# Kernel tuning notes

Measured on AMD Instinct MI355X. Metric: run time of the kernel, lower is better.

Reference implementation:

```python
import jax, jax.numpy as jnp
import numpy as np

B, S, DM, DC, L, NS = 4, 2048, 2048, 512, 4, 5  # batch, seq, d_model, d_cortical, n_layers, n_settle


def _ln(x, g, b):
    # torch nn.LayerNorm, eps=1e-5
    m = x.mean(-1, keepdims=True)
    v = ((x - m) ** 2).mean(-1, keepdims=True)
    return (x - m) * jax.lax.rsqrt(v + 1e-5) * g + b


def setup_inputs() -> dict:
    key = jax.random.key(0)
    ks = jax.random.split(key, 20)
    f = lambda k, sh: jax.random.normal(k, sh, jnp.float32) * 0.02
    return dict(
        qwen_final_hidden=jax.random.normal(ks[0], (B, S, DM), jnp.float32),
        obs=jax.random.normal(ks[1], (4, B, S, DM), jnp.float32),
        proj_W=f(ks[2], (4, DC, DM)), proj_b=f(ks[3], (4, DC)),
        fuse_W=f(ks[4], (DC, 4 * DC)), fuse_b=f(ks[5], (DC,)),
        up_W=f(ks[6], (L, DC, DC)), up_b=f(ks[7], (L, DC)),
        lateral_W=f(ks[8], (L, DC, DC)), lateral_b=f(ks[9], (L, DC)),
        precision_logit=f(ks[10], (L, DC)),
        ln_g=jnp.ones((L, DC), jnp.float32), ln_b=jnp.zeros((L, DC), jnp.float32),
        down_W=f(ks[11], (L - 1, DC, DC)), down_b=f(ks[12], (L - 1, DC)),
        out1_W=f(ks[13], (DC, DC)), out1_b=f(ks[14], (DC,)),
        out2_W=f(ks[15], (DM, DC)), out2_b=f(ks[16], (DM,)),
    )


def reference(qwen_final_hidden, obs, proj_W, proj_b, fuse_W, fuse_b,
              up_W, up_b, lateral_W, lateral_b, precision_logit,
              ln_g, ln_b, down_W, down_b, out1_W, out1_b, out2_W, out2_b):
    b, s, dm = qwen_final_hidden.shape
    # per-observed-layer input projections, concatenated along features
    proj = jnp.einsum('obsd,ocd->bsoc', obs, proj_W) + proj_b  # (B,S,4,DC)
    cat = proj.reshape(b, s, -1)
    fused = cat @ fuse_W.T + fuse_b                             # (B,S,DC)
    x0 = fused.reshape(b * s, DC)                               # per-token cortical input

    prec = jax.nn.sigmoid(precision_logit)                      # (L,DC)

    # initial bottom-up pass: activations = compress(x)
    acts = []
    x = x0
    for i in range(L):
        x = _ln(x @ up_W[i].T + up_b[i], ln_g[i], ln_b[i])
        acts.append(x)

    # settling iterations
    for _ in range(NS):
        # top-down predictions computed from pre-sweep activations
        preds = [None] * L
        for i in range(L - 1, 0, -1):
            if i < L - 1:  # top layer has no top-down weights
                preds[i - 1] = acts[i] @ down_W[i].T + down_b[i]
        x = x0
        for i in range(L):
            compressed = _ln(x @ up_W[i].T + up_b[i], ln_g[i], ln_b[i])
            target = preds[i] if preds[i] is not None else acts[i]
            werr = (compressed - target) * prec[i]
            lateral = acts[i] @ lateral_W[i].T + lateral_b[i]
            acts[i] = _ln(acts[i] + 0.5 * werr + 0.1 * lateral, ln_g[i], ln_b[i])
            x = acts[i]

    top = acts[-1]
    h = jax.nn.gelu(top @ out1_W.T + out1_b, approximate=False)
    correction = (h @ out2_W.T + out2_b).reshape(b, s, dm)
    return qwen_final_hidden + correction
```

## Files before the change

### kernel.cpp

```cpp
#include <hip/hip_runtime.h>
#include <hip/hip_bf16.h>
#include <math.h>

#define NTOK 8192
#define DMD  2048
#define DCC  512
#define TOKH 4194304

typedef __attribute__((ext_vector_type(8))) short short8;
typedef __attribute__((ext_vector_type(4))) float f32x4;

__device__ inline float bf2f(unsigned short u) {
    union { unsigned int i; float f; } x; x.i = ((unsigned int)u) << 16; return x.f;
}
__device__ inline unsigned short f2bf(float f) {
    union { float f; unsigned int i; } x; x.f = f;
    unsigned int u = x.i;
    return (unsigned short)((u + 0x7fffu + ((u >> 16) & 1u)) >> 16);
}

typedef const __attribute__((address_space(1))) unsigned int* gas1_t;
typedef __attribute__((address_space(3))) unsigned int* las3_t;
__device__ inline void async16(const void* g, void* l) {
    __builtin_amdgcn_global_load_lds(
        (gas1_t)g,
        (las3_t)(unsigned int)(unsigned long long)l, 16, 0, 0);
}

#define VMCNT(N) asm volatile("s_waitcnt vmcnt(" #N ")" ::: "memory")

__global__ __launch_bounds__(256)
void cvt_kernel(const float* __restrict__ s, unsigned short* __restrict__ d, int n4)
{
    for (int i = blockIdx.x * 256 + threadIdx.x; i < n4; i += gridDim.x * 256) {
        float4 v = ((const float4*)s)[i];
        ushort4 o;
        o.x = f2bf(v.x); o.y = f2bf(v.y); o.z = f2bf(v.z); o.w = f2bf(v.w);
        ((ushort4*)d)[i] = o;
    }
}

struct PrepArgs {
    const float* wsrc[6];
    const float* proj_W;
    const float* fuse_W;
    const float* fuse_b;
    const float* proj_b;
    unsigned short* wdst;
    unsigned short* projT;
    float* bp;
};

__global__ __launch_bounds__(256)
void prep_kernel(PrepArgs pa)
{
    __shared__ float t[32][33];
    const int bid = blockIdx.x;
    const int tid = threadIdx.x;

    if (bid < 2048) {
        const int total = 1310720;
        for (int i = bid * 256 + tid; i < total; i += 2048 * 256) {
            const float* sp; int base;
            if      (i <  262144) { sp = pa.wsrc[0]; base = 0;       }
            else if (i <  524288) { sp = pa.wsrc[1]; base = 262144;  }
            else if (i <  786432) { sp = pa.wsrc[2]; base = 524288;  }
            else if (i <  983040) { sp = pa.wsrc[3]; base = 786432;  }
            else if (i < 1048576) { sp = pa.wsrc[4]; base = 983040;  }
            else                  { sp = pa.wsrc[5]; base = 1048576; }
            float4 v = ((const float4*)sp)[i - base];
            ushort4 o;
            o.x = f2bf(v.x); o.y = f2bf(v.y); o.z = f2bf(v.z); o.w = f2bf(v.w);
            ((ushort4*)pa.wdst)[i] = o;
        }
    } else if (bid < 6144) {
        const int b2  = bid - 2048;
        const int o   = b2 >> 10;
        const int rem = b2 & 1023;
        const int jb  = (rem & 63) * 32;
        const int kb  = (rem >> 6) * 32;
        const int r   = tid >> 3;
        const int c4  = (tid & 7) * 4;
        {
            const float* s = pa.proj_W + ((size_t)o * DCC + kb + r) * DMD + jb + c4;
            float4 v = *(const float4*)s;
            t[r][c4+0]=v.x; t[r][c4+1]=v.y; t[r][c4+2]=v.z; t[r][c4+3]=v.w;
        }
        __syncthreads();
        {
            ushort4 u;
            u.x = f2bf(t[c4+0][r]); u.y = f2bf(t[c4+1][r]);
            u.z = f2bf(t[c4+2][r]); u.w = f2bf(t[c4+3][r]);
            *(ushort4*)(pa.projT + ((size_t)o * DMD + jb + r) * DCC + kb + c4) = u;
        }
    } else {
        const int b3  = bid - 6144;
        const int row = b3 * 8 + (tid >> 5);
        const int l32 = tid & 31;
        const float* r = pa.fuse_W + (size_t)row * (4 * DCC) + l32 * 64;
        const float* p = pa.proj_b + l32 * 64;
        float s = 0.f;
        #pragma unroll
        for (int k = 0; k < 64; k += 4) {
            float4 v = *(const float4*)(r + k);
            float4 q = *(const float4*)(p + k);
            s += v.x*q.x + v.y*q.y + v.z*q.z + v.w*q.w;
        }
        #pragma unroll
        for (int off = 16; off; off >>= 1) s += __shfl_xor(s, off, 64);
        if (l32 == 0) pa.bp[row] = s + pa.fuse_b[row];
    }
}

struct GArgs {
    const unsigned short* A[6];
    const unsigned short* W[6];
    const float*          bias[6];
    const float*          add[6];
    void*                 C[6];
};

template<bool OUTF32, bool GELU>
__global__ __launch_bounds__(256)
void gemm16(GArgs ga, int lda, int ldw, int ldadd, int ldc, int K)
{
    __shared__ unsigned short As[3][128 * 32];
    __shared__ unsigned short Bs[3][128 * 32];

    const int z    = blockIdx.z;
    const int tid  = threadIdx.x;
    const int wave = tid >> 6;
    const int lane = tid & 63;

    const int nwg   = gridDim.x * gridDim.y;
    const int bid   = blockIdx.y * gridDim.x + blockIdx.x;
    const int swz   = (bid & 7) * (nwg >> 3) + (bid >> 3);
    const int bn    = (swz % gridDim.x) * 128;
    const int bm    = (swz / gridDim.x) * 128;

    const int wr   = wave >> 1;
    const int wc   = wave & 1;

    const unsigned short* Ap = ga.A[z];
    const unsigned short* Wp = ga.W[z];

    const int lrow = lane >> 2;
    const int lcol = (lane & 3) * 8;
    const int l15  = lane & 15;
    const int lh   = lane >> 4;

    f32x4 acc[4][4] = {};

    const int nsteps = K >> 5;

    auto issue = [&](int buf, int k0) {
        #pragma unroll
        for (int r = 0; r < 2; ++r) {
            int c = wave + r * 4;
            async16(Ap + (size_t)(bm + c * 16 + lrow) * lda + k0 + lcol,
                    &As[buf][c * 512]);
            async16(Wp + (size_t)(bn + c * 16 + lrow) * ldw + k0 + lcol,
                    &Bs[buf][c * 512]);
        }
    };

    issue(0, 0);
    issue(1, 32);

    for (int t = 0; t < nsteps; ++t) {
        const int cur = t % 3;
        if (t < nsteps - 1) VMCNT(4);
        else                VMCNT(0);
        __builtin_amdgcn_s_barrier();
        if (t + 2 < nsteps) issue((t + 2) % 3, (t + 2) * 32);

        short8 af[4], bfr[4];
        #pragma unroll
        for (int i = 0; i < 4; ++i) {
            af[i]  = *(const short8*)&As[cur][(wr * 64 + i * 16 + l15) * 32 + lh * 8];
            bfr[i] = *(const short8*)&Bs[cur][(wc * 64 + i * 16 + l15) * 32 + lh * 8];
        }
        __builtin_amdgcn_s_setprio(1);
        #pragma unroll
        for (int mi = 0; mi < 4; ++mi)
            #pragma unroll
            for (int ni = 0; ni < 4; ++ni)
                acc[mi][ni] = __builtin_amdgcn_mfma_f32_16x16x32_bf16(
                    af[mi], bfr[ni], acc[mi][ni], 0, 0, 0);
        __builtin_amdgcn_s_setprio(0);
    }

    const float* bias = ga.bias[z];
    const float* add  = ga.add[z];
    #pragma unroll
    for (int ni = 0; ni < 4; ++ni) {
        int col = bn + wc * 64 + ni * 16 + l15;
        float bv = bias ? bias[col] : 0.0f;
        #pragma unroll
        for (int mi = 0; mi < 4; ++mi) {
            #pragma unroll
            for (int r = 0; r < 4; ++r) {
                int row = bm + wr * 64 + mi * 16 + lh * 4 + r;
                float vv = acc[mi][ni][r] + bv;
                if (GELU) vv = 0.5f * vv * (1.0f + erff(vv * 0.7071067811865475f));
                if (OUTF32) {
                    if (add) vv += add[(size_t)row * ldadd + col];
                    ((float*)ga.C[z])[(size_t)row * ldc + col] = vv;
                } else {
                    ((unsigned short*)ga.C[z])[(size_t)row * ldc + col] = f2bf(vv);
                }
            }
        }
    }
}

__global__ __launch_bounds__(256)
void x0red(const float* __restrict__ partial, const float* __restrict__ bp,
           unsigned short* __restrict__ x0)
{
    const int i = blockIdx.x * 256 + threadIdx.x;
    float4 a = ((const float4*)partial)[i];
    float4 b = ((const float4*)(partial + TOKH))[i];
    float4 c = ((const float4*)(partial + 2 * (size_t)TOKH))[i];
    float4 d = ((const float4*)(partial + 3 * (size_t)TOKH))[i];
    const int col = (i * 4) & (DCC - 1);
    float4 bv = *(const float4*)(bp + col);
    ushort4 o;
    o.x = f2bf(a.x + b.x + c.x + d.x + bv.x);
    o.y = f2bf(a.y + b.y + c.y + d.y + bv.y);
    o.z = f2bf(a.z + b.z + c.z + d.z + bv.z);
    o.w = f2bf(a.w + b.w + c.w + d.w + bv.w);
    ((ushort4*)x0)[i] = o;
}

__device__ inline int csw(int rl, int col) {
    int s = ((rl >> 2) & 3) ^ (rl & 3);
    return rl * 512 + (col ^ (s << 4));
}

template<int MODE>
__global__ __launch_bounds__(512)
void gemm_fused2(const unsigned short* __restrict__ Ap,
                 const unsigned short* __restrict__ W0,
                 const float* __restrict__ bias0,
                 const float* __restrict__ g0,
                 const float* __restrict__ b0,
                 const unsigned short* a0,
                 const unsigned short* t0,
                 const unsigned short* __restrict__ lat0,
                 const float* __restrict__ logit0,
                 unsigned short* out0,
                 const unsigned short* __restrict__ W1,
                 const float* __restrict__ bias1,
                 const float* __restrict__ g1,
                 const float* __restrict__ b1,
                 const unsigned short* a1,
                 const unsigned short* t1,
                 const unsigned short* __restrict__ lat1,
                 const float* __restrict__ logit1,
                 unsigned short* out1)
{
    __shared__ unsigned short Bs[3][512 * 32];
    __shared__ unsigned short As3[3][32 * 32];
    __shared__ unsigned short xS[32 * 512];
    __shared__ float red[2][8][32];

    const int tid  = threadIdx.x;
    const int wave = tid >> 6;
    const int lane = tid & 63;
    const int lrow = lane >> 2;
    const int lc8  = (lane & 3) * 8;
    const int bm   = blockIdx.x * 32;
    const int l15  = lane & 15;
    const int lh   = lane >> 4;
    const int c0   = lane * 8;

    f32x4 acc[2][4];

    auto ln1_to_xS = [&](const float* bias, const float* g, const float* b) {
        float bv[4], gv[4], bbv[4];
        #pragma unroll
        for (int ni = 0; ni < 4; ++ni) {
            int col = wave * 64 + ni * 16 + l15;
            bv[ni] = bias[col]; gv[ni] = g[col]; bbv[ni] = b[col];
        }
        float ps[2][4], pq[2][4];
        #pragma unroll
        for (int mi = 0; mi < 2; ++mi)
            #pragma unroll
            for (int rr = 0; rr < 4; ++rr) {
                float s = 0.f, q = 0.f;
                #pragma unroll
                for (int ni = 0; ni < 4; ++ni) {
                    float v = acc[mi][ni][rr] + bv[ni];
                    acc[mi][ni][rr] = v;
                    s += v; q += v * v;
                }
                #pragma unroll
                for (int off = 1; off < 16; off <<= 1) {
                    s += __shfl_xor(s, off, 64);
                    q += __shfl_xor(q, off, 64);
                }
                ps[mi][rr] = s; pq[mi][rr] = q;
            }
        if (l15 == 0) {
            #pragma unroll
            for (int mi = 0; mi < 2; ++mi)
                #pragma unroll
                for (int rr = 0; rr < 4; ++rr) {
                    int rl = mi * 16 + lh * 4 + rr;
                    red[0][wave][rl] = ps[mi][rr];
                    red[1][wave][rl] = pq[mi][rr];
                }
        }
        __syncthreads();
        #pragma unroll
        for (int mi = 0; mi < 2; ++mi)
            #pragma unroll
            for (int rr = 0; rr < 4; ++rr) {
                int rl = mi * 16 + lh * 4 + rr;
                float s = 0.f, q = 0.f;
                #pragma unroll
                for (int w = 0; w < 8; ++w) { s += red[0][w][rl]; q += red[1][w][rl]; }
                float m1 = s * (1.0f / DCC);
                float r1 = rsqrtf(q * (1.0f / DCC) - m1 * m1 + 1e-5f);
                #pragma unroll
                for (int ni = 0; ni < 4; ++ni) {
                    int col = wave * 64 + ni * 16 + l15;
                    xS[csw(rl, col)] = f2bf((acc[mi][ni][rr] - m1) * r1 * gv[ni] + bbv[ni]);
                }
            }
        __syncthreads();
    };

    auto phase2 = [&](const unsigned short* a_in, const unsigned short* t_in,
                      const unsigned short* lat_in, const float* g,
                      const float* b, const float* logit,
                      unsigned short* outp, bool keep) {
        if constexpr (MODE == 0) {
            #pragma unroll
            for (int rr = 0; rr < 4; ++rr) {
                const int rl = wave * 4 + rr;
                const size_t gbase = (size_t)(bm + rl) * DCC + c0;
                short8 cm = *(const short8*)&xS[csw(rl, c0)];
                *(short8*)(outp + gbase) = cm;
            }
        } else {
            float gr[8], br[8], pr[8];
            {
                float4 ga = *(const float4*)(g + c0),     gb = *(const float4*)(g + c0 + 4);
                float4 ba = *(const float4*)(b + c0),     bb2 = *(const float4*)(b + c0 + 4);
                float4 pA = *(const float4*)(logit + c0), pB = *(const float4*)(logit + c0 + 4);
                float gt[8] = {ga.x,ga.y,ga.z,ga.w,gb.x,gb.y,gb.z,gb.w};
                float bt[8] = {ba.x,ba.y,ba.z,ba.w,bb2.x,bb2.y,bb2.z,bb2.w};
                float pt[8] = {pA.x,pA.y,pA.z,pA.w,pB.x,pB.y,pB.z,pB.w};
                #pragma unroll
                for (int j = 0; j < 8; ++j) {
                    gr[j] = gt[j]; br[j] = bt[j];
                    pr[j] = 1.0f / (1.0f + __expf(-pt[j]));
                }
            }
            #pragma unroll
            for (int rr = 0; rr < 4; ++rr) {
                const int rl = wave * 4 + rr;
                const size_t gbase = (size_t)(bm + rl) * DCC + c0;
                short8 cm = *(const short8*)&xS[csw(rl, c0)];
                short8 ar = *(const short8*)(a_in + gbase);
                short8 tr = *(const short8*)(t_in + gbase);
                short8 lr = *(const short8*)(lat_in + gbase);
                float tv[8], s = 0.f, q = 0.f;
                #pragma unroll
                for (int j = 0; j < 8; ++j) {
                    float val = bf2f((unsigned short)ar[j])
                              + 0.5f * (bf2f((unsigned short)cm[j]) - bf2f((unsigned short)tr[j])) * pr[j]
                              + 0.1f * bf2f((unsigned short)lr[j]);
                    tv[j] = val; s += val; q += val * val;
                }
                #pragma unroll
                for (int off = 1; off < 64; off <<= 1) {
                    s += __shfl_xor(s, off, 64);
                    q += __shfl_xor(q, off, 64);
                }
                float m2 = s * (1.0f / DCC);
                float r2 = rsqrtf(q * (1.0f / DCC) - m2 * m2 + 1e-5f);
                short8 o;
                #pragma unroll
                for (int j = 0; j < 8; ++j)
                    o[j] = (short)f2bf((tv[j] - m2) * r2 * gr[j] + br[j]);
                *(short8*)(outp + gbase) = o;
                if (keep) *(short8*)&xS[csw(rl, c0)] = o;
            }
        }
    };

    #pragma unroll
    for (int mi = 0; mi < 2; ++mi)
        #pragma unroll
        for (int ni = 0; ni < 4; ++ni)
            acc[mi][ni] = f32x4{0.f, 0.f, 0.f, 0.f};

    auto issueA = [&](int buf, int k0) {
        if (wave < 2)
            async16(Ap + (size_t)(bm + wave * 16 + lrow) * DCC + k0 + lc8,
                    &As3[buf][wave * 512]);
        #pragma unroll
        for (int r = 0; r < 4; ++r)
            async16(W0 + (size_t)((r * 8 + wave) * 16 + lrow) * DCC + k0 + lc8,
                    &Bs[buf][(r * 8 + wave) * 512]);
    };

    issueA(0, 0);
    issueA(1, 32);

    #pragma unroll
    for (int t = 0; t < 16; ++t) {
        const int cur = t % 3;
        if (t < 15) { if (wave < 2) VMCNT(5); else VMCNT(4); }
        else        { VMCNT(0); }
        __builtin_amdgcn_s_barrier();
        if (t + 2 < 16) issueA((t + 2) % 3, (t + 2) * 32);

        short8 af[2], bfr[4];
        #pragma unroll
        for (int mi = 0; mi < 2; ++mi)
            af[mi] = *(const short8*)&As3[cur][(mi * 16 + l15) * 32 + lh * 8];
        #pragma unroll
        for (int ni = 0; ni < 4; ++ni)
            bfr[ni] = *(const short8*)&Bs[cur][(wave * 64 + ni * 16 + l15) * 32 + lh * 8];
        __builtin_amdgcn_s_setprio(1);
        #pragma unroll
        for (int mi = 0; mi < 2; ++mi)
            #pragma unroll
            for (int ni = 0; ni < 4; ++ni)
                acc[mi][ni] = __builtin_amdgcn_mfma_f32_16x16x32_bf16(
                    af[mi], bfr[ni], acc[mi][ni], 0, 0, 0);
        __builtin_amdgcn_s_setprio(0);
    }

    ln1_to_xS(bias0, g0, b0);
    phase2(a0, t0, lat0, g0, b0, logit0, out0, true);
    __syncthreads();

    #pragma unroll
    for (int mi = 0; mi < 2; ++mi)
        #pragma unroll
        for (int ni = 0; ni < 4; ++ni)
            acc[mi][ni] = f32x4{0.f, 0.f, 0.f, 0.f};

    auto issueB = [&](int buf, int k0) {
        #pragma unroll
        for (int r = 0; r < 4; ++r)
            async16(W1 + (size_t)((r * 8 + wave) * 16 + lrow) * DCC + k0 + lc8,
                    &Bs[buf][(r * 8 + wave) * 512]);
    };

    issueB(0, 0);
    issueB(1, 32);

    #pragma unroll
    for (int t = 0; t < 16; ++t) {
        const int cur = t % 3;
        if (t < 15) VMCNT(4);
        else        VMCNT(0);
        __builtin_amdgcn_s_barrier();
        if (t + 2 < 16) issueB((t + 2) % 3, (t + 2) * 32);

        short8 af[2], bfr[4];
        #pragma unroll
        for (int mi = 0; mi < 2; ++mi)
            af[mi] = *(const short8*)&xS[csw(mi * 16 + l15, t * 32 + lh * 8)];
        #pragma unroll
        for (int ni = 0; ni < 4; ++ni)
            bfr[ni] = *(const short8*)&Bs[cur][(wave * 64 + ni * 16 + l15) * 32 + lh * 8];
        __builtin_amdgcn_s_setprio(1);
        #pragma unroll
        for (int mi = 0; mi < 2; ++mi)
            #pragma unroll
            for (int ni = 0; ni < 4; ++ni)
                acc[mi][ni] = __builtin_amdgcn_mfma_f32_16x16x32_bf16(
                    af[mi], bfr[ni], acc[mi][ni], 0, 0, 0);
        __builtin_amdgcn_s_setprio(0);
    }

    ln1_to_xS(bias1, g1, b1);
    phase2(a1, t1, lat1, g1, b1, logit1, out1, false);
}

extern "C" void kernel_launch(void* const* d_in, const int* in_sizes, int n_in,
                              void* d_out, int out_size, void* d_ws, size_t ws_size,
                              hipStream_t stream)
{
    const float* qwen   = (const float*)d_in[0];
    const float* obs    = (const float*)d_in[1];
    const float* proj_W = (const float*)d_in[2];
    const float* proj_b = (const float*)d_in[3];
    const float* fuse_W = (const float*)d_in[4];
    const float* fuse_b = (const float*)d_in[5];
    const float* up_W   = (const float*)d_in[6];
    const float* up_b   = (const float*)d_in[7];
    const float* lat_W  = (const float*)d_in[8];
    const float* lat_b  = (const float*)d_in[9];
    const float* plogit = (const float*)d_in[10];
    const float* ln_g   = (const float*)d_in[11];
    const float* ln_b   = (const float*)d_in[12];
    const float* down_W = (const float*)d_in[13];
    const float* down_b = (const float*)d_in[14];
    const float* out1_W = (const float*)d_in[15];
    const float* out1_b = (const float*)d_in[16];
    const float* out2_W = (const float*)d_in[17];
    const float* out2_b = (const float*)d_in[18];
    float* out = (float*)d_out;

    unsigned short* wsu = (unsigned short*)d_ws;
    float*          bp     = (float*)wsu;
    unsigned short* h16    = wsu + 2048;
    unsigned short* M16    = wsu + 8388608;
    unsigned short* x0b    = wsu + 16777216;
    unsigned short* acts16[4] = {
        wsu + 20971520, wsu + 20971520 + TOKH,
        wsu + 20971520 + 2 * TOKH, wsu + 20971520 + 3 * TOKH };
    unsigned short* w16    = wsu + 37748736;
    unsigned short* fuseW16 = w16;
    unsigned short* upW16   = w16 + 1048576;
    unsigned short* latW16  = w16 + 2097152;
    unsigned short* downW16 = w16 + 3145728;
    unsigned short* out1W16 = w16 + 3932160;
    unsigned short* out2W16 = w16 + 4194304;
    unsigned short* projT16 = wsu + 47185920;
    unsigned short* obs16   = wsu + 47185920;

    float*          part32  = (float*)d_out;
    unsigned short* outu = (unsigned short*)d_out;
    unsigned short* pred16a = outu;
    unsigned short* pred16b = outu + TOKH;
    unsigned short* lat16[4] = { outu + 2*TOKH, outu + 3*TOKH, outu + 4*TOKH, outu + 5*TOKH };

    dim3 blk(256);
    dim3 blk512(512);

    {
        PrepArgs pa;
        pa.wsrc[0] = fuse_W; pa.wsrc[1] = up_W;   pa.wsrc[2] = lat_W;
        pa.wsrc[3] = down_W; pa.wsrc[4] = out1_W; pa.wsrc[5] = out2_W;
        pa.proj_W = proj_W; pa.fuse_W = fuse_W; pa.fuse_b = fuse_b;
        pa.proj_b = proj_b;
        pa.wdst = w16; pa.projT = projT16; pa.bp = bp;
        prep_kernel<<<dim3(6208), blk, 0, stream>>>(pa);
    }

    {
        GArgs a{};
        for (int o = 0; o < 4; ++o) {
            a.A[o] = fuseW16 + o * DCC;
            a.W[o] = projT16 + (size_t)o * DMD * DCC;
            a.bias[o] = nullptr;
            a.C[o] = M16 + (size_t)o * DCC * DMD;
        }
        gemm16<false, false><<<dim3(DMD/128, DCC/128, 4), blk, 0, stream>>>(
            a, 4 * DCC, DCC, 0, DMD, DCC);
    }

    cvt_kernel<<<dim3(4096), blk, 0, stream>>>(obs, obs16, 16777216);

    {
        GArgs a{};
        for (int o = 0; o < 4; ++o) {
            a.A[o] = obs16 + (size_t)o * NTOK * DMD;
            a.W[o] = M16 + (size_t)o * DCC * DMD;
            a.bias[o] = nullptr;
            a.add[o]  = nullptr;
            a.C[o] = part32 + (size_t)o * TOKH;
        }
        gemm16<true, false><<<dim3(DCC/128, NTOK/128, 4), blk, 0, stream>>>(
            a, DMD, DMD, 0, DCC, DMD);
    }
    x0red<<<dim3(TOKH/4/256), blk, 0, stream>>>(part32, bp, x0b);

    dim3 fgrid(NTOK / 32);

    gemm_fused2<0><<<fgrid, blk512, 0, stream>>>(
        x0b,
        upW16,                 up_b,           ln_g,           ln_b,
        nullptr, nullptr, nullptr, nullptr, acts16[0],
        upW16 + 262144,        up_b + DCC,     ln_g + DCC,     ln_b + DCC,
        nullptr, nullptr, nullptr, nullptr, acts16[1]);
    gemm_fused2<0><<<fgrid, blk512, 0, stream>>>(
        acts16[1],
        upW16 + 2 * 262144,    up_b + 2 * DCC, ln_g + 2 * DCC, ln_b + 2 * DCC,
        nullptr, nullptr, nullptr, nullptr, acts16[2],
        upW16 + 3 * 262144,    up_b + 3 * DCC, ln_g + 3 * DCC, ln_b + 3 * DCC,
        nullptr, nullptr, nullptr, nullptr, acts16[3]);

    for (int s = 0; s < 5; ++s) {
        {
            GArgs a{};
            a.A[0] = acts16[1]; a.W[0] = downW16 + (size_t)1 * DCC * DCC;
            a.bias[0] = down_b + 1 * DCC; a.C[0] = pred16a;
            a.A[1] = acts16[2]; a.W[1] = downW16 + (size_t)2 * DCC * DCC;
            a.bias[1] = down_b + 2 * DCC; a.C[1] = pred16b;
            for (int i = 0; i < 4; ++i) {
                a.A[2 + i] = acts16[i];
                a.W[2 + i] = latW16 + (size_t)i * DCC * DCC;
                a.bias[2 + i] = lat_b + i * DCC;
                a.C[2 + i] = lat16[i];
            }
            gemm16<false, false><<<dim3(DCC/128, NTOK/128, 6), blk, 0, stream>>>(
                a, DCC, DCC, 0, DCC, DCC);
        }
        gemm_fused2<1><<<fgrid, blk512, 0, stream>>>(
            x0b,
            upW16,              up_b,           ln_g,           ln_b,
            acts16[0], pred16a, lat16[0], plogit,         acts16[0],
            upW16 + 262144,     up_b + DCC,     ln_g + DCC,     ln_b + DCC,
            acts16[1], pred16b, lat16[1], plogit + DCC,   acts16[1]);
        gemm_fused2<1><<<fgrid, blk512, 0, stream>>>(
            acts16[1],
            upW16 + 2 * 262144, up_b + 2 * DCC, ln_g + 2 * DCC, ln_b + 2 * DCC,
            acts16[2], acts16[2], lat16[2], plogit + 2 * DCC, acts16[2],
            upW16 + 3 * 262144, up_b + 3 * DCC, ln_g + 3 * DCC, ln_b + 3 * DCC,
            acts16[3], acts16[3], lat16[3], plogit + 3 * DCC, acts16[3]);
    }

    {
        GArgs a{};
        a.A[0] = acts16[3]; a.W[0] = out1W16; a.bias[0] = out1_b; a.C[0] = h16;
        gemm16<false, true><<<dim3(DCC/128, NTOK/128, 1), blk, 0, stream>>>(
            a, DCC, DCC, 0, DCC, DCC);
    }
    {
        GArgs a{};
        a.A[0] = h16; a.W[0] = out2W16; a.bias[0] = out2_b;
        a.add[0] = qwen; a.C[0] = out;
        gemm16<true, false><<<dim3(DMD/128, NTOK/128, 1), blk, 0, stream>>>(
            a, DCC, DCC, DMD, DMD, DCC);
    }
}
```

Baseline: 1.351 ms.

## Fuse all four up-layer GEMM+LayerNorm stages into one kernel per sweep

Replaces the two two-layer fused kernels with a single kernel that chains all four layers. Each layer's normalized output stays in shared memory as the next layer's A operand. This removes one launch per sweep and the global write/read of the layer-1 activations between kernels. The cost is longer per-block serial work. The layer loop is not unrolled, so the per-layer pointers are read from a struct at runtime.

```diff
diff --git a/kernel.cpp b/kernel.cpp
--- a/kernel.cpp
+++ b/kernel.cpp
@@ -6,6 +6,7 @@
 #define DMD  2048
 #define DCC  512
 #define TOKH 4194304
+#define WSZ  262144
 
 typedef __attribute__((ext_vector_type(8))) short short8;
 typedef __attribute__((ext_vector_type(4))) float f32x4;
@@ -238,27 +239,21 @@
     return rl * 512 + (col ^ (s << 4));
 }
 
+struct FArgs {
+    const unsigned short* W[4];
+    const float*          bias[4];
+    const float*          g[4];
+    const float*          b[4];
+    const unsigned short* a[4];
+    const unsigned short* t[4];
+    const unsigned short* lat[4];
+    const float*          logit[4];
+    unsigned short*       outp[4];
+};
+
 template<int MODE>
 __global__ __launch_bounds__(512)
-void gemm_fused2(const unsigned short* __restrict__ Ap,
-                 const unsigned short* __restrict__ W0,
-                 const float* __restrict__ bias0,
-                 const float* __restrict__ g0,
-                 const float* __restrict__ b0,
-                 const unsigned short* a0,
-                 const unsigned short* t0,
-                 const unsigned short* __restrict__ lat0,
-                 const float* __restrict__ logit0,
-                 unsigned short* out0,
-                 const unsigned short* __restrict__ W1,
-                 const float* __restrict__ bias1,
-                 const float* __restrict__ g1,
-                 const float* __restrict__ b1,
-                 const unsigned short* a1,
-                 const unsigned short* t1,
-                 const unsigned short* __restrict__ lat1,
-                 const float* __restrict__ logit1,
-                 unsigned short* out1)
+void gemm_fused4(const unsigned short* __restrict__ Ap, FArgs fa)
 {
     __shared__ unsigned short Bs[3][512 * 32];
     __shared__ unsigned short As3[3][32 * 32];
@@ -277,7 +272,10 @@
 
     f32x4 acc[2][4];
 
-    auto ln1_to_xS = [&](const float* bias, const float* g, const float* b) {
+    auto ln1_to_xS = [&](int li) {
+        const float* bias = fa.bias[li];
+        const float* g    = fa.g[li];
+        const float* b    = fa.b[li];
         float bv[4], gv[4], bbv[4];
         #pragma unroll
         for (int ni = 0; ni < 4; ++ni) {
@@ -333,10 +331,8 @@
         __syncthreads();
     };
 
-    auto phase2 = [&](const unsigned short* a_in, const unsigned short* t_in,
-                      const unsigned short* lat_in, const float* g,
-                      const float* b, const float* logit,
-                      unsigned short* outp, bool keep) {
+    auto phase2 = [&](int li, bool keep) {
+        unsigned short* outp = fa.outp[li];
         if constexpr (MODE == 0) {
             #pragma unroll
             for (int rr = 0; rr < 4; ++rr) {
@@ -346,6 +342,9 @@
                 *(short8*)(outp + gbase) = cm;
             }
         } else {
+            const float* g     = fa.g[li];
+            const float* b     = fa.b[li];
+            const float* logit = fa.logit[li];
             float gr[8], br[8], pr[8];
             {
                 float4 ga = *(const float4*)(g + c0),     gb = *(const float4*)(g + c0 + 4);
@@ -360,6 +359,9 @@
                     pr[j] = 1.0f / (1.0f + __expf(-pt[j]));
                 }
             }
+            const unsigned short* a_in   = fa.a[li];
+            const unsigned short* t_in   = fa.t[li];
+            const unsigned short* lat_in = fa.lat[li];
             #pragma unroll
             for (int rr = 0; rr < 4; ++rr) {
                 const int rl = wave * 4 + rr;
@@ -399,91 +401,99 @@
         for (int ni = 0; ni < 4; ++ni)
             acc[mi][ni] = f32x4{0.f, 0.f, 0.f, 0.f};
 
-    auto issueA = [&](int buf, int k0) {
-        if (wave < 2)
-            async16(Ap + (size_t)(bm + wave * 16 + lrow) * DCC + k0 + lc8,
-                    &As3[buf][wave * 512]);
-        #pragma unroll
-        for (int r = 0; r < 4; ++r)
-            async16(W0 + (size_t)((r * 8 + wave) * 16 + lrow) * DCC + k0 + lc8,
-                    &Bs[buf][(r * 8 + wave) * 512]);
-    };
-
-    issueA(0, 0);
-    issueA(1, 32);
-
-    #pragma unroll
-    for (int t = 0; t < 16; ++t) {
-        const int cur = t % 3;
-        if (t < 15) { if (wave < 2) VMCNT(5); else VMCNT(4); }
-        else        { VMCNT(0); }
-        __builtin_amdgcn_s_barrier();
-        if (t + 2 < 16) issueA((t + 2) % 3, (t + 2) * 32);
-
-        short8 af[2], bfr[4];
+    {
+        const unsigned short* W0 = fa.W[0];
+        auto issueA = [&](int buf, int k0) {
+            if (wave < 2)
+                async16(Ap + (size_t)(bm + wave * 16 + lrow) * DCC + k0 + lc8,
+                        &As3[buf][wave * 512]);
+            #pragma unroll
+            for (int r = 0; r < 4; ++r)
+                async16(W0 + (size_t)((r * 8 + wave) * 16 + lrow) * DCC + k0 + lc8,
+                        &Bs[buf][(r * 8 + wave) * 512]);
+        };
+
+        issueA(0, 0);
+        issueA(1, 32);
+
+        #pragma unroll
+        for (int t = 0; t < 16; ++t) {
+            const int cur = t % 3;
+            if (t < 15) { if (wave < 2) VMCNT(5); else VMCNT(4); }
+            else        { VMCNT(0); }
+            __builtin_amdgcn_s_barrier();
+            if (t + 2 < 16) issueA((t + 2) % 3, (t + 2) * 32);
+
+            short8 af[2], bfr[4];
+            #pragma unroll
+            for (int mi = 0; mi < 2; ++mi)
+                af[mi] = *(const short8*)&As3[cur][(mi * 16 + l15) * 32 + lh * 8];
+            #pragma unroll
+            for (int ni = 0; ni < 4; ++ni)
+                bfr[ni] = *(const short8*)&Bs[cur][(wave * 64 + ni * 16 + l15) * 32 + lh * 8];
+            __builtin_amdgcn_s_setprio(1);
+            #pragma unroll
+            for (int mi = 0; mi < 2; ++mi)
+                #pragma unroll
+                for (int ni = 0; ni < 4; ++ni)
+                    acc[mi][ni] = __builtin_amdgcn_mfma_f32_16x16x32_bf16(
+                        af[mi], bfr[ni], acc[mi][ni], 0, 0, 0);
+            __builtin_amdgcn_s_setprio(0);
+        }
+    }
+
+    ln1_to_xS(0);
+    phase2(0, true);
+    __syncthreads();
+
+    #pragma unroll 1
+    for (int li = 1; li < 4; ++li) {
         #pragma unroll
         for (int mi = 0; mi < 2; ++mi)
-            af[mi] = *(const short8*)&As3[cur][(mi * 16 + l15) * 32 + lh * 8];
-        #pragma unroll
-        for (int ni = 0; ni < 4; ++ni)
-            bfr[ni] = *(const short8*)&Bs[cur][(wave * 64 + ni * 16 + l15) * 32 + lh * 8];
-        __builtin_amdgcn_s_setprio(1);
-        #pragma unroll
-        for (int mi = 0; mi < 2; ++mi)
             #pragma unroll
             for (int ni = 0; ni < 4; ++ni)
-                acc[mi][ni] = __builtin_amdgcn_mfma_f32_16x16x32_bf16(
-                    af[mi], bfr[ni], acc[mi][ni], 0, 0, 0);
-        __builtin_amdgcn_s_setprio(0);
-    }
-
-    ln1_to_xS(bias0, g0, b0);
-    phase2(a0, t0, lat0, g0, b0, logit0, out0, true);
-    __syncthreads();
-
-    #pragma unroll
-    for (int mi = 0; mi < 2; ++mi)
-        #pragma unroll
-        for (int ni = 0; ni < 4; ++ni)
-            acc[mi][ni] = f32x4{0.f, 0.f, 0.f, 0.f};
-
-    auto issueB = [&](int buf, int k0) {
-        #pragma unroll
-        for (int r = 0; r < 4; ++r)
-            async16(W1 + (size_t)((r * 8 + wave) * 16 + lrow) * DCC + k0 + lc8,
-                    &Bs[buf][(r * 8 + wave) * 512]);
-    };
-
-    issueB(0, 0);
-    issueB(1, 32);
-
-    #pragma unroll
-    for (int t = 0; t < 16; ++t) {
-        const int cur = t % 3;
-        if (t < 15) VMCNT(4);
-        else        VMCNT(0);
-        __builtin_amdgcn_s_barrier();
-        if (t + 2 < 16) issueB((t + 2) % 3, (t + 2) * 32);
-
-        short8 af[2], bfr[4];
-        #pragma unroll
-        for (int mi = 0; mi < 2; ++mi)
-            af[mi] = *(const short8*)&xS[csw(mi * 16 + l15, t * 32 + lh * 8)];
-        #pragma unroll
-        for (int ni = 0; ni < 4; ++ni)
-            bfr[ni] = *(const short8*)&Bs[cur][(wave * 64 + ni * 16 + l15) * 32 + lh * 8];
-        __builtin_amdgcn_s_setprio(1);
-        #pragma unroll
-        for (int mi = 0; mi < 2; ++mi)
+                acc[mi][ni] = f32x4{0.f, 0.f, 0.f, 0.f};
+
+        const unsigned short* W1 = fa.W[li];
+        auto issueB = [&](int buf, int k0) {
+            #pragma unroll
+            for (int r = 0; r < 4; ++r)
+                async16(W1 + (size_t)((r * 8 + wave) * 16 + lrow) * DCC + k0 + lc8,
+                        &Bs[buf][(r * 8 + wave) * 512]);
+        };
+
+        issueB(0, 0);
+        issueB(1, 32);
+
+        #pragma unroll
+        for (int t = 0; t < 16; ++t) {
+            const int cur = t % 3;
+            if (t < 15) VMCNT(4);
+            else        VMCNT(0);
+            __builtin_amdgcn_s_barrier();
+            if (t + 2 < 16) issueB((t + 2) % 3, (t + 2) * 32);
+
+            short8 af[2], bfr[4];
+            #pragma unroll
+            for (int mi = 0; mi < 2; ++mi)
+                af[mi] = *(const short8*)&xS[csw(mi * 16 + l15, t * 32 + lh * 8)];
             #pragma unroll
             for (int ni = 0; ni < 4; ++ni)
-                acc[mi][ni] = __builtin_amdgcn_mfma_f32_16x16x32_bf16(
-                    af[mi], bfr[ni], acc[mi][ni], 0, 0, 0);
-        __builtin_amdgcn_s_setprio(0);
-    }
-
-    ln1_to_xS(bias1, g1, b1);
-    phase2(a1, t1, lat1, g1, b1, logit1, out1, false);
+                bfr[ni] = *(const short8*)&Bs[cur][(wave * 64 + ni * 16 + l15) * 32 + lh * 8];
+            __builtin_amdgcn_s_setprio(1);
+            #pragma unroll
+            for (int mi = 0; mi < 2; ++mi)
+                #pragma unroll
+                for (int ni = 0; ni < 4; ++ni)
+                    acc[mi][ni] = __builtin_amdgcn_mfma_f32_16x16x32_bf16(
+                        af[mi], bfr[ni], acc[mi][ni], 0, 0, 0);
+            __builtin_amdgcn_s_setprio(0);
+        }
+
+        ln1_to_xS(li);
+        phase2(li, li < 3);
+        if (li < 3) __syncthreads();
+    }
 }
 
 extern "C" void kernel_launch(void* const* d_in, const int* in_sizes, int n_in,
@@ -578,18 +588,17 @@
 
     dim3 fgrid(NTOK / 32);
 
-    gemm_fused2<0><<<fgrid, blk512, 0, stream>>>(
-        x0b,
-        upW16,                 up_b,           ln_g,           ln_b,
-        nullptr, nullptr, nullptr, nullptr, acts16[0],
-        upW16 + 262144,        up_b + DCC,     ln_g + DCC,     ln_b + DCC,
-        nullptr, nullptr, nullptr, nullptr, acts16[1]);
-    gemm_fused2<0><<<fgrid, blk512, 0, stream>>>(
-        acts16[1],
-        upW16 + 2 * 262144,    up_b + 2 * DCC, ln_g + 2 * DCC, ln_b + 2 * DCC,
-        nullptr, nullptr, nullptr, nullptr, acts16[2],
-        upW16 + 3 * 262144,    up_b + 3 * DCC, ln_g + 3 * DCC, ln_b + 3 * DCC,
-        nullptr, nullptr, nullptr, nullptr, acts16[3]);
+    {
+        FArgs fa{};
+        for (int i = 0; i < 4; ++i) {
+            fa.W[i]    = upW16 + (size_t)i * WSZ;
+            fa.bias[i] = up_b + i * DCC;
+            fa.g[i]    = ln_g + i * DCC;
+            fa.b[i]    = ln_b + i * DCC;
+            fa.outp[i] = acts16[i];
+        }
+        gemm_fused4<0><<<fgrid, blk512, 0, stream>>>(x0b, fa);
+    }
 
     for (int s = 0; s < 5; ++s) {
         {
@@ -607,18 +616,24 @@
             gemm16<false, false><<<dim3(DCC/128, NTOK/128, 6), blk, 0, stream>>>(
                 a, DCC, DCC, 0, DCC, DCC);
         }
-        gemm_fused2<1><<<fgrid, blk512, 0, stream>>>(
-            x0b,
-            upW16,              up_b,           ln_g,           ln_b,
-            acts16[0], pred16a, lat16[0], plogit,         acts16[0],
-            upW16 + 262144,     up_b + DCC,     ln_g + DCC,     ln_b + DCC,
-            acts16[1], pred16b, lat16[1], plogit + DCC,   acts16[1]);
-        gemm_fused2<1><<<fgrid, blk512, 0, stream>>>(
-            acts16[1],
-            upW16 + 2 * 262144, up_b + 2 * DCC, ln_g + 2 * DCC, ln_b + 2 * DCC,
-            acts16[2], acts16[2], lat16[2], plogit + 2 * DCC, acts16[2],
-            upW16 + 3 * 262144, up_b + 3 * DCC, ln_g + 3 * DCC, ln_b + 3 * DCC,
-            acts16[3], acts16[3], lat16[3], plogit + 3 * DCC, acts16[3]);
+        {
+            FArgs fa{};
+            for (int i = 0; i < 4; ++i) {
+                fa.W[i]     = upW16 + (size_t)i * WSZ;
+                fa.bias[i]  = up_b + i * DCC;
+                fa.g[i]     = ln_g + i * DCC;
+                fa.b[i]     = ln_b + i * DCC;
+                fa.a[i]     = acts16[i];
+                fa.lat[i]   = lat16[i];
+                fa.logit[i] = plogit + i * DCC;
+                fa.outp[i]  = acts16[i];
+            }
+            fa.t[0] = pred16a;
+            fa.t[1] = pred16b;
+            fa.t[2] = acts16[2];
+            fa.t[3] = acts16[3];
+            gemm_fused4<1><<<fgrid, blk512, 0, stream>>>(x0b, fa);
+        }
     }
 
     {
```

New measurement: 1.354 ms. No clear change (+0.2%).
